# Optimization experiments

Measured on AMD Instinct MI355X. Metric: run time of the kernel, lower is better.

Reference implementation:

```python
import jax, jax.numpy as jnp
import numpy as np

N_NODES = 100000
N_EDGES = 3200000
D_IN = 128
D_OUT = 128


def setup_inputs() -> dict:
    key = jax.random.key(0)
    ks = jax.random.split(key, 7)
    x = jax.random.normal(ks[0], (N_NODES, D_IN), dtype=jnp.float32)
    weight = jax.random.normal(ks[1], (D_IN, D_OUT), dtype=jnp.float32) * (1.0 / np.sqrt(D_OUT))
    bias = jax.random.normal(ks[2], (D_OUT,), dtype=jnp.float32) * (1.0 / np.sqrt(D_OUT))
    adj_rows = jax.random.randint(ks[3], (N_EDGES,), 0, N_NODES, dtype=jnp.int32)
    adj_cols = jax.random.randint(ks[4], (N_EDGES,), 0, N_NODES, dtype=jnp.int32)
    adj_vals = jax.random.uniform(ks[5], (N_EDGES,), dtype=jnp.float32)
    # norm kept in [0.5, 1.5) to avoid division blow-up (degree-like normalizer)
    norm = jax.random.uniform(ks[6], (N_NODES, 1), dtype=jnp.float32) + 0.5
    return {"x": x, "weight": weight, "bias": bias,
            "adj_rows": adj_rows, "adj_cols": adj_cols, "adj_vals": adj_vals,
            "norm": norm}


def reference(x, weight, bias, adj_rows, adj_cols, adj_vals, norm):
    # support = input @ W               [N, D_OUT]
    support = x @ weight
    # output = spmm(adj, support): gather source rows, scale by edge value,
    # scatter-add into destination rows.
    gathered = support[adj_cols] * adj_vals[:, None]          # [E, D_OUT]
    output = jax.ops.segment_sum(gathered, adj_rows, num_segments=x.shape[0])
    output = output / norm
    return output + bias
```

## Files before the change

kernel.cpp:

```cpp
#include <hip/hip_runtime.h>

#define M_NODES 100000
#define N_EDGES 3200000
#define D 128
#define NBUCK 1563
#define FILL_CHUNK 12288
#define FILL_BLOCKS 261
#define GEMM_BLOCKS 782
#define PREP_BLOCKS (FILL_BLOCKS + GEMM_BLOCKS)
#define BUCK_CAP 4096
#define NSEG 7

#define OFF_SUP16  0ull
#define OFF_BCNT   25600000ull
#define OFF_REC    25608192ull
#define WS_NEEDED  76824576ull

__device__ __forceinline__ unsigned short f2bf(float f) {
    unsigned u = __float_as_uint(f);
    u += 0x7fff + ((u >> 16) & 1);
    return (unsigned short)(u >> 16);
}
__device__ __forceinline__ float2 bfpair(unsigned u) {
    float2 r;
    r.x = __uint_as_float(u << 16);
    r.y = __uint_as_float(u & 0xffff0000u);
    return r;
}

__global__ __launch_bounds__(512) void prep_kernel(const float* __restrict__ x,
                                                   const float* __restrict__ w,
                                                   unsigned* __restrict__ sup16,
                                                   const int* __restrict__ rows,
                                                   const int* __restrict__ cols,
                                                   const float* __restrict__ vals,
                                                   int* __restrict__ bcnt,
                                                   int2* __restrict__ rec,
                                                   int M) {
    __shared__ __align__(16) char smem[37120];
    const int tid = threadIdx.x;

    if (blockIdx.x < FILL_BLOCKS) {
        int* cnt = (int*)smem;
        int* bas = (int*)(smem + 6256);
        unsigned short* lrank = (unsigned short*)(smem + 12512);
        for (int i = tid; i < NBUCK; i += 512) cnt[i] = 0;
        __syncthreads();
        const long long base = (long long)blockIdx.x * FILL_CHUNK;

#pragma unroll
        for (int i = 0; i < 6; ++i) {
            const int li = (i * 512 + tid) * 4;
            const long long e = base + li;
            if (e < N_EDGES) {
                const int4 r = *(const int4*)&rows[e];
                lrank[li + 0] = (unsigned short)atomicAdd(&cnt[r.x >> 6], 1);
                lrank[li + 1] = (unsigned short)atomicAdd(&cnt[r.y >> 6], 1);
                lrank[li + 2] = (unsigned short)atomicAdd(&cnt[r.z >> 6], 1);
                lrank[li + 3] = (unsigned short)atomicAdd(&cnt[r.w >> 6], 1);
            }
        }
        __syncthreads();
        for (int i = tid; i < NBUCK; i += 512)
            bas[i] = cnt[i] ? atomicAdd(&bcnt[i], cnt[i]) : 0;
        __syncthreads();
#pragma unroll
        for (int i = 0; i < 6; ++i) {
            const int li = (i * 512 + tid) * 4;
            const long long e = base + li;
            if (e < N_EDGES) {
                const int4   r = *(const int4*)&rows[e];
                const int4   c = *(const int4*)&cols[e];
                const float4 v = *(const float4*)&vals[e];
                int p;
                p = bas[r.x >> 6] + lrank[li + 0];
                if (p < BUCK_CAP)
                    rec[(size_t)(r.x >> 6) * BUCK_CAP + p] =
                        make_int2(c.x | ((r.x & 63) << 20), __float_as_int(v.x));
                p = bas[r.y >> 6] + lrank[li + 1];
                if (p < BUCK_CAP)
                    rec[(size_t)(r.y >> 6) * BUCK_CAP + p] =
                        make_int2(c.y | ((r.y & 63) << 20), __float_as_int(v.y));
                p = bas[r.z >> 6] + lrank[li + 2];
                if (p < BUCK_CAP)
                    rec[(size_t)(r.z >> 6) * BUCK_CAP + p] =
                        make_int2(c.z | ((r.z & 63) << 20), __float_as_int(v.z));
                p = bas[r.w >> 6] + lrank[li + 3];
                if (p < BUCK_CAP)
                    rec[(size_t)(r.w >> 6) * BUCK_CAP + p] =
                        make_int2(c.w | ((r.w & 63) << 20), __float_as_int(v.w));
            }
        }
        return;
    }

    float (*sX)[128] = (float(*)[128])smem;
    float (*sW)[128] = (float(*)[128])(smem + 16384);

    const int r0 = (blockIdx.x - FILL_BLOCKS) * 128;
    const int tx = tid & 31;
    const int ty = tid >> 5;

    float acc[8][4];
#pragma unroll
    for (int r = 0; r < 8; ++r)
#pragma unroll
        for (int c = 0; c < 4; ++c) acc[r][c] = 0.f;

    for (int c0 = 0; c0 < 128; c0 += 32) {
        {
            const int row = tid >> 3;
            const int kk  = (tid & 7) * 4;
#pragma unroll
            for (int h = 0; h < 2; ++h) {
                const int rr = row + h * 64;
                float4 v = make_float4(0.f, 0.f, 0.f, 0.f);
                if (r0 + rr < M)
                    v = *(const float4*)&x[(size_t)(r0 + rr) * D + c0 + kk];
                sX[kk + 0][rr] = v.x;
                sX[kk + 1][rr] = v.y;
                sX[kk + 2][rr] = v.z;
                sX[kk + 3][rr] = v.w;
            }
        }
#pragma unroll
        for (int i = tid; i < 1024; i += 512) {
            const int k  = i >> 5;
            const int c4 = (i & 31) * 4;
            *(float4*)&sW[k][c4] = *(const float4*)&w[(size_t)(c0 + k) * D + c4];
        }
        __syncthreads();

#pragma unroll
        for (int k = 0; k < 32; ++k) {
            const float4 wv = *(const float4*)&sW[k][tx * 4];
            const float4 xa = *(const float4*)&sX[k][ty * 8];
            const float4 xb = *(const float4*)&sX[k][ty * 8 + 4];
            const float xr[8] = {xa.x, xa.y, xa.z, xa.w, xb.x, xb.y, xb.z, xb.w};
#pragma unroll
            for (int r = 0; r < 8; ++r) {
                acc[r][0] += xr[r] * wv.x;
                acc[r][1] += xr[r] * wv.y;
                acc[r][2] += xr[r] * wv.z;
                acc[r][3] += xr[r] * wv.w;
            }
        }
        __syncthreads();
    }

#pragma unroll
    for (int r = 0; r < 8; ++r) {
        const int row = r0 + ty * 8 + r;
        if (row < M) {
            uint2 p;
            p.x = (unsigned)f2bf(acc[r][0]) | ((unsigned)f2bf(acc[r][1]) << 16);
            p.y = (unsigned)f2bf(acc[r][2]) | ((unsigned)f2bf(acc[r][3]) << 16);
            *(uint2*)&sup16[(size_t)row * 64 + tx * 2] = p;
        }
    }
}

__global__ __launch_bounds__(512) void gather_kernel(const unsigned* __restrict__ sup16,
                                                     const int* __restrict__ bcnt,
                                                     const int2* __restrict__ rec,
                                                     const float* __restrict__ norm,
                                                     const float* __restrict__ bias,
                                                     float* __restrict__ out) {
    __shared__ int2 elist[BUCK_CAP];
    __shared__ int cnt[512];
    __shared__ int rbase[514];
    const int tid = threadIdx.x;
    const int b   = blockIdx.x;

    cnt[tid] = 0;
    __syncthreads();
    const int n = min(bcnt[b], BUCK_CAP);
    const int2* __restrict__ recb = rec + (size_t)b * BUCK_CAP;

    for (int k = tid; k < n; k += 512) {
        const int ex = recb[k].x;
        const int key = (((ex & 0xFFFFF) >> 14) << 6) | ((ex >> 20) & 63);
        atomicAdd(&cnt[key], 1);
    }
    __syncthreads();
    int* tsum = (int*)elist;
    const int myc = cnt[tid];
    tsum[tid] = myc;
    __syncthreads();
    for (int off = 1; off < 512; off <<= 1) {
        const int v = (tid >= off) ? tsum[tid - off] : 0;
        __syncthreads();
        tsum[tid] += v;
        __syncthreads();
    }
    const int excl = tsum[tid] - myc;
    rbase[tid] = excl;
    cnt[tid]   = excl;
    if (tid == 0) rbase[512] = n;
    __syncthreads();
    for (int k = tid; k < n; k += 512) {
        const int2 e = recb[k];
        const int key = (((e.x & 0xFFFFF) >> 14) << 6) | ((e.x >> 20) & 63);
        const int p = atomicAdd(&cnt[key], 1);
        elist[p] = make_int2(e.x & 0xFFFFF, e.y);
    }
    __syncthreads();

    const int w    = tid >> 6;
    const int lane = tid & 63;
    const unsigned* __restrict__ supl = sup16 + lane;
    const int fo = lane * 2;
    const float2 b2 = *(const float2*)&bias[fo];

    float2 acc[8];
#pragma unroll
    for (int r = 0; r < 8; ++r) acc[r] = make_float2(0.f, 0.f);

#pragma unroll 1
    for (int seg = 0; seg < NSEG; ++seg) {
        const int kbase = seg * 64 + w * 8;
#pragma unroll
        for (int rr = 0; rr < 8; ++rr) {
            int j = rbase[kbase + rr];
            const int j1 = rbase[kbase + rr + 1];
            float2 a = acc[rr];
            for (; j + 4 <= j1; j += 4) {
                int2 e[4];
#pragma unroll
                for (int q = 0; q < 4; ++q) e[q] = elist[j + q];
                unsigned u[4];
#pragma unroll
                for (int q = 0; q < 4; ++q) u[q] = supl[(unsigned)e[q].x << 6];
#pragma unroll
                for (int q = 0; q < 4; ++q) {
                    const float v = __int_as_float(e[q].y);
                    const float2 p = bfpair(u[q]);
                    a.x = fmaf(p.x, v, a.x);
                    a.y = fmaf(p.y, v, a.y);
                }
            }
            for (; j < j1; ++j) {
                const int2 e = elist[j];
                const unsigned u = supl[(unsigned)e.x << 6];
                const float v = __int_as_float(e.y);
                const float2 p = bfpair(u);
                a.x = fmaf(p.x, v, a.x);
                a.y = fmaf(p.y, v, a.y);
            }
            acc[rr] = a;
        }
    }

#pragma unroll
    for (int rr = 0; rr < 8; ++rr) {
        const int row = b * 64 + w * 8 + rr;
        if (row < M_NODES) {
            const float inv = 1.0f / norm[row];
            float2 o;
            o.x = fmaf(acc[rr].x, inv, b2.x);
            o.y = fmaf(acc[rr].y, inv, b2.y);
            *(float2*)&out[(size_t)row * D + fo] = o;
        }
    }
}

__global__ __launch_bounds__(256) void gemm32_kernel(const float* __restrict__ x,
                                                     const float* __restrict__ w,
                                                     float* __restrict__ support,
                                                     int M) {
    __shared__ float sX[32][64];
    __shared__ float sW[32][128];
    const int tid = threadIdx.x;
    const int r0  = blockIdx.x * 64;
    const int tx  = tid & 31;
    const int ty  = tid >> 5;
    float acc[8][4];
#pragma unroll
    for (int r = 0; r < 8; ++r)
#pragma unroll
        for (int c = 0; c < 4; ++c) acc[r][c] = 0.f;
    for (int c0 = 0; c0 < 128; c0 += 32) {
        {
            const int row = tid >> 3;
            const int kk  = (tid & 7) * 4;
#pragma unroll
            for (int h = 0; h < 2; ++h) {
                const int rr = row + h * 32;
                float4 v = make_float4(0.f, 0.f, 0.f, 0.f);
                if (r0 + rr < M)
                    v = *(const float4*)&x[(size_t)(r0 + rr) * D + c0 + kk];
                sX[kk + 0][rr] = v.x; sX[kk + 1][rr] = v.y;
                sX[kk + 2][rr] = v.z; sX[kk + 3][rr] = v.w;
            }
        }
#pragma unroll
        for (int i = tid; i < 1024; i += 256) {
            const int k  = i >> 5;
            const int c4 = (i & 31) * 4;
            *(float4*)&sW[k][c4] = *(const float4*)&w[(size_t)(c0 + k) * D + c4];
        }
        __syncthreads();
#pragma unroll
        for (int k = 0; k < 32; ++k) {
            const float4 wv = *(const float4*)&sW[k][tx * 4];
            const float4 xa = *(const float4*)&sX[k][ty * 8];
            const float4 xb = *(const float4*)&sX[k][ty * 8 + 4];
            const float xr[8] = {xa.x, xa.y, xa.z, xa.w, xb.x, xb.y, xb.z, xb.w};
#pragma unroll
            for (int r = 0; r < 8; ++r) {
                acc[r][0] += xr[r] * wv.x; acc[r][1] += xr[r] * wv.y;
                acc[r][2] += xr[r] * wv.z; acc[r][3] += xr[r] * wv.w;
            }
        }
        __syncthreads();
    }
#pragma unroll
    for (int r = 0; r < 8; ++r) {
        const int row = r0 + ty * 8 + r;
        if (row < M)
            *(float4*)&support[(size_t)row * D + tx * 4] =
                make_float4(acc[r][0], acc[r][1], acc[r][2], acc[r][3]);
    }
}

__global__ __launch_bounds__(256) void spmm_kernel(const float* __restrict__ support,
                                                   const int* __restrict__ rows,
                                                   const int* __restrict__ cols,
                                                   const float* __restrict__ vals,
                                                   float* __restrict__ out) {
    const long long t = (long long)blockIdx.x * 256 + threadIdx.x;
    const int e = (int)(t >> 5);
    if (e >= N_EDGES) return;
    const int f   = (int)(t & 31) * 4;
    const int src = cols[e];
    const int dst = rows[e];
    const float v = vals[e];
    const float4 s = *(const float4*)&support[(size_t)src * D + f];
    float* o = &out[(size_t)dst * D + f];
    atomicAdd(o + 0, s.x * v);
    atomicAdd(o + 1, s.y * v);
    atomicAdd(o + 2, s.z * v);
    atomicAdd(o + 3, s.w * v);
}

__global__ __launch_bounds__(256) void finalize_kernel(float* __restrict__ out,
                                                       const float* __restrict__ norm,
                                                       const float* __restrict__ bias) {
    const int t = blockIdx.x * 256 + threadIdx.x;
    const int nrow = t >> 5;
    if (nrow >= M_NODES) return;
    const int f = (t & 31) * 4;
    const float inv = 1.0f / norm[nrow];
    float4 o = *(float4*)&out[(size_t)nrow * D + f];
    const float4 b = *(const float4*)&bias[f];
    o.x = o.x * inv + b.x; o.y = o.y * inv + b.y;
    o.z = o.z * inv + b.z; o.w = o.w * inv + b.w;
    *(float4*)&out[(size_t)nrow * D + f] = o;
}

extern "C" void kernel_launch(void* const* d_in, const int* in_sizes, int n_in,
                              void* d_out, int out_size, void* d_ws, size_t ws_size,
                              hipStream_t stream) {
    const float* x    = (const float*)d_in[0];
    const float* w    = (const float*)d_in[1];
    const float* bias = (const float*)d_in[2];
    const int*   rows = (const int*)d_in[3];
    const int*   cols = (const int*)d_in[4];
    const float* vals = (const float*)d_in[5];
    const float* norm = (const float*)d_in[6];
    float* out = (float*)d_out;
    char* ws = (char*)d_ws;

    if (ws_size >= WS_NEEDED) {
        unsigned* sup16 = (unsigned*)(ws + OFF_SUP16);
        int*      bcnt  = (int*)(ws + OFF_BCNT);
        int2*     rec   = (int2*)(ws + OFF_REC);

        hipMemsetAsync(bcnt, 0, NBUCK * sizeof(int), stream);
        prep_kernel<<<PREP_BLOCKS, 512, 0, stream>>>(x, w, sup16, rows, cols, vals,
                                                     bcnt, rec, M_NODES);
        gather_kernel<<<NBUCK, 512, 0, stream>>>(sup16, bcnt, rec,
                                                 norm, bias, out);
    } else {
        float* support = (float*)ws;
        gemm32_kernel<<<(M_NODES + 63) / 64, 256, 0, stream>>>(x, w, support, M_NODES);
        hipMemsetAsync(d_out, 0, (size_t)out_size * sizeof(float), stream);
        const long long spmm_threads = (long long)N_EDGES * 32;
        spmm_kernel<<<(int)((spmm_threads + 255) / 256), 256, 0, stream>>>(support, rows, cols, vals, out);
        finalize_kernel<<<(M_NODES * 32 + 255) / 256, 256, 0, stream>>>(out, norm, bias);
    }
}
```

Measured before the change: 331.6 us.

## Interleave gathers across eight rows and cache bucket records in registers

The gather loop now walks all eight destination rows of a wavefront in lockstep, issuing up to sixteen independent bf16 support loads per iteration instead of four loads from one row at a time. This is meant to raise memory-level parallelism and hide gather latency. Separately, each thread keeps its bucket records and keys in registers between the counting pass and the scatter pass, so the records are not read from global memory twice. The trade-off is higher register pressure and predicated loads when row lengths differ, since iterations run to the longest row in the segment.

```diff
diff --git a/kernel.cpp b/kernel.cpp
--- a/kernel.cpp
+++ b/kernel.cpp
@@ -177,10 +177,16 @@
     const int n = min(bcnt[b], BUCK_CAP);
     const int2* __restrict__ recb = rec + (size_t)b * BUCK_CAP;
 
-    for (int k = tid; k < n; k += 512) {
-        const int ex = recb[k].x;
-        const int key = (((ex & 0xFFFFF) >> 14) << 6) | ((ex >> 20) & 63);
-        atomicAdd(&cnt[key], 1);
+    int2 myE[8];
+    int  keys[8];
+#pragma unroll
+    for (int i = 0; i < 8; ++i) {
+        const int k = tid + i * 512;
+        if (k < n) {
+            myE[i] = recb[k];
+            keys[i] = ((((unsigned)myE[i].x & 0xFFFFF) >> 14) << 6) | ((myE[i].x >> 20) & 63);
+            atomicAdd(&cnt[keys[i]], 1);
+        }
     }
     __syncthreads();
     int* tsum = (int*)elist;
@@ -198,11 +204,13 @@
     cnt[tid]   = excl;
     if (tid == 0) rbase[512] = n;
     __syncthreads();
-    for (int k = tid; k < n; k += 512) {
-        const int2 e = recb[k];
-        const int key = (((e.x & 0xFFFFF) >> 14) << 6) | ((e.x >> 20) & 63);
-        const int p = atomicAdd(&cnt[key], 1);
-        elist[p] = make_int2(e.x & 0xFFFFF, e.y);
+#pragma unroll
+    for (int i = 0; i < 8; ++i) {
+        const int k = tid + i * 512;
+        if (k < n) {
+            const int p = atomicAdd(&cnt[keys[i]], 1);
+            elist[p] = make_int2(myE[i].x & 0xFFFFF, myE[i].y);
+        }
     }
     __syncthreads();
 
@@ -218,42 +226,47 @@
 
 #pragma unroll 1
     for (int seg = 0; seg < NSEG; ++seg) {
-        const int kbase = seg * 64 + w * 8;
-#pragma unroll
-        for (int rr = 0; rr < 8; ++rr) {
-            int j = rbase[kbase + rr];
-            const int j1 = rbase[kbase + rr + 1];
-            float2 a = acc[rr];
-            for (; j + 4 <= j1; j += 4) {
-                int2 e[4];
-#pragma unroll
-                for (int q = 0; q < 4; ++q) e[q] = elist[j + q];
-                unsigned u[4];
-#pragma unroll
-                for (int q = 0; q < 4; ++q) u[q] = supl[(unsigned)e[q].x << 6];
-#pragma unroll
-                for (int q = 0; q < 4; ++q) {
-                    const float v = __int_as_float(e[q].y);
-                    const float2 p = bfpair(u[q]);
-                    a.x = fmaf(p.x, v, a.x);
-                    a.y = fmaf(p.y, v, a.y);
+        const int kbase = seg * 64 + (w << 3);
+        int js[8], ln[8];
+        int len = 0;
+#pragma unroll
+        for (int r = 0; r < 8; ++r) {
+            js[r] = __builtin_amdgcn_readfirstlane(rbase[kbase + r]);
+            const int e1 = __builtin_amdgcn_readfirstlane(rbase[kbase + r + 1]);
+            ln[r] = e1 - js[r];
+            len = max(len, ln[r]);
+        }
+#pragma unroll 1
+        for (int it = 0; it < len; it += 2) {
+            unsigned u[16];
+#pragma unroll
+            for (int r = 0; r < 8; ++r) {
+                if (it < ln[r])
+                    u[2 * r]     = supl[(unsigned)elist[js[r] + it].x << 6];
+                if (it + 1 < ln[r])
+                    u[2 * r + 1] = supl[(unsigned)elist[js[r] + it + 1].x << 6];
+            }
+#pragma unroll
+            for (int r = 0; r < 8; ++r) {
+                if (it < ln[r]) {
+                    const float v = __int_as_float(elist[js[r] + it].y);
+                    const float2 p = bfpair(u[2 * r]);
+                    acc[r].x = fmaf(p.x, v, acc[r].x);
+                    acc[r].y = fmaf(p.y, v, acc[r].y);
                 }
-            }
-            for (; j < j1; ++j) {
-                const int2 e = elist[j];
-                const unsigned u = supl[(unsigned)e.x << 6];
-                const float v = __int_as_float(e.y);
-                const float2 p = bfpair(u);
-                a.x = fmaf(p.x, v, a.x);
-                a.y = fmaf(p.y, v, a.y);
-            }
-            acc[rr] = a;
+                if (it + 1 < ln[r]) {
+                    const float v = __int_as_float(elist[js[r] + it + 1].y);
+                    const float2 p = bfpair(u[2 * r + 1]);
+                    acc[r].x = fmaf(p.x, v, acc[r].x);
+                    acc[r].y = fmaf(p.y, v, acc[r].y);
+                }
+            }
         }
     }
 
 #pragma unroll
     for (int rr = 0; rr < 8; ++rr) {
-        const int row = b * 64 + w * 8 + rr;
+        const int row = b * 64 + (w << 3) + rr;
         if (row < M_NODES) {
             const float inv = 1.0f / norm[row];
             float2 o;
```

After: 425.5 us. 1.28x slower.
